# Optimization experiments

Measured on AMD Instinct MI355X. Metric: run time of the kernel, lower is better.

Reference implementation:

```python
import jax, jax.numpy as jnp
import numpy as np

B, C, H, W = 16, 256, 64, 64

def setup_inputs() -> dict:
    key = jax.random.key(0)
    ks = jax.random.split(key, 4)
    scale = 1.0 / np.sqrt(C)
    return {
        "x": jax.random.normal(ks[0], (B, C, H, W), dtype=jnp.float32),
        "w1": jax.random.normal(ks[1], (C, C), dtype=jnp.float32) * scale,
        "b1": jnp.zeros((C,), dtype=jnp.float32),
        "w2": jax.random.normal(ks[2], (C, C), dtype=jnp.float32) * scale,
        "b2": jnp.zeros((C,), dtype=jnp.float32),
        "w3": jax.random.normal(ks[3], (C, C), dtype=jnp.float32) * scale,
        "b3": jnp.zeros((C,), dtype=jnp.float32),
    }

def reference(x, w1, b1, w2, b2, w3, b3):
    b, c, h, w = x.shape
    n = h * w
    # 1x1 convs == per-pixel linear maps over channels; w has shape [C_out, C_in]
    def proj(wt, bias):
        return jnp.einsum('bchw,oc->bohw', x, wt) + bias[None, :, None, None]
    v = proj(w1, b1).reshape(b, c, n).transpose(0, 2, 1)   # [B, N, C]
    q = proj(w2, b2).reshape(b, c, n)                      # [B, C, N]
    k = proj(w3, b3).reshape(b, c, n)                      # [B, C, N]
    weight = jnp.einsum('bcn,bdn->bcd', q, k)              # [B, C, C]
    # global softmax over the entire flattened C*C matrix per batch element
    weight = jax.nn.softmax(weight.reshape(b, -1), axis=1).reshape(b, c, c)
    out = jnp.einsum('bnc,bcd->bdn', v, weight)            # [B, C, N]
    return out.reshape(x.shape)
```

## Files before the change

### kernel.cpp

```cpp
#include <hip/hip_runtime.h>


typedef unsigned short u16;
typedef __attribute__((ext_vector_type(8))) short short8;
typedef __attribute__((ext_vector_type(4))) float floatx4;

__device__ __forceinline__ u16 f2b(float f) {
  union { float f; unsigned int u; } v; v.f = f;
  unsigned int u = v.u;
  return (u16)((u + 0x7fffu + ((u >> 16) & 1u)) >> 16);
}
__device__ __forceinline__ float b2f(u16 h) {
  union { unsigned int u; float f; } v; v.u = ((unsigned int)h) << 16;
  return v.f;
}

__global__ __launch_bounds__(256) void prep_w_kernel(
    const float* __restrict__ w1, const float* __restrict__ w2, const float* __restrict__ w3,
    u16* __restrict__ W1Th, u16* __restrict__ W2h, u16* __restrict__ W2l,
    u16* __restrict__ W3h, u16* __restrict__ W3l) {
  const int blk = blockIdx.x, t = threadIdx.x;
  if (blk < 64) {
    __shared__ float tile[32][33];
    const int e0 = (blk & 7) * 32, c0 = (blk >> 3) * 32;
    const int tx = t & 31, ty = t >> 5;
#pragma unroll
    for (int i = 0; i < 4; ++i)
      tile[ty + i * 8][tx] = w1[(c0 + ty + i * 8) * 256 + e0 + tx];
    __syncthreads();
#pragma unroll
    for (int i = 0; i < 4; ++i)
      W1Th[(e0 + ty + i * 8) * 256 + c0 + tx] = f2b(tile[tx][ty + i * 8]);
  } else {
    const int i = (blk - 64) * 256 + t;
    const int e = i & 0xffff;
    const float f = (i >> 16) ? w3[e] : w2[e];
    u16 h = f2b(f);
    if (i >> 16) { W3h[e] = h; W3l[e] = f2b(f - b2f(h)); }
    else         { W2h[e] = h; W2l[e] = f2b(f - b2f(h)); }
  }
}

__global__ __launch_bounds__(512, 2) void gram_kernel(
    const float* __restrict__ x, float* __restrict__ Gp, float* __restrict__ xsum) {
  constexpr int LR = 40;
  __shared__ u16 lH[256 * LR], lL[256 * LR];
  const int b = blockIdx.x >> 4, s = blockIdx.x & 15;
  const float* Xb = x + (long)b * 1048576 + s * 256;
  const int t = threadIdx.x;
  const int lane = t & 63, wave = t >> 6;
  const int quad = lane >> 4, l16 = lane & 15;
  const int wm = (wave & 1) * 128, wn = (wave >> 1) * 64;
  floatx4 acc[8][4] = {};
  float xacc[2] = {0.f, 0.f};
  for (int kb = 0; kb < 256; kb += 32) {
    __syncthreads();
#pragma unroll
    for (int h = 0; h < 2; ++h) {
      const int item = t + h * 512;
      const int r = item >> 2, qc = (item & 3) * 8;
      const float4 f0 = *(const float4*)(Xb + (long)r * 4096 + kb + qc);
      const float4 f1 = *(const float4*)(Xb + (long)r * 4096 + kb + qc + 4);
      const float f[8] = {f0.x, f0.y, f0.z, f0.w, f1.x, f1.y, f1.z, f1.w};
      union { u16 h8[8]; uint4 q; } uh, ul;
#pragma unroll
      for (int i = 0; i < 8; ++i) {
        const u16 hi = f2b(f[i]);
        uh.h8[i] = hi;
        ul.h8[i] = f2b(f[i] - b2f(hi));
        xacc[h] += f[i];
      }
      *(uint4*)(lH + r * LR + qc) = uh.q;
      *(uint4*)(lL + r * LR + qc) = ul.q;
    }
    __syncthreads();
    short8 ah[8], al[8];
#pragma unroll
    for (int i = 0; i < 8; ++i) {
      ah[i] = *(const short8*)(lH + (wm + i * 16 + l16) * LR + quad * 8);
      al[i] = *(const short8*)(lL + (wm + i * 16 + l16) * LR + quad * 8);
    }
#pragma unroll
    for (int j = 0; j < 4; ++j) {
      const short8 bh = *(const short8*)(lH + (wn + j * 16 + l16) * LR + quad * 8);
      const short8 bl = *(const short8*)(lL + (wn + j * 16 + l16) * LR + quad * 8);
#pragma unroll
      for (int i = 0; i < 8; ++i) {
        acc[i][j] = __builtin_amdgcn_mfma_f32_16x16x32_bf16(ah[i], bh, acc[i][j], 0, 0, 0);
        acc[i][j] = __builtin_amdgcn_mfma_f32_16x16x32_bf16(ah[i], bl, acc[i][j], 0, 0, 0);
        acc[i][j] = __builtin_amdgcn_mfma_f32_16x16x32_bf16(al[i], bh, acc[i][j], 0, 0, 0);
      }
    }
  }
#pragma unroll
  for (int h = 0; h < 2; ++h) {
    float v = xacc[h];
    v += __shfl_xor(v, 1);
    v += __shfl_xor(v, 2);
    if ((t & 3) == 0) atomicAdd(&xsum[b * 256 + ((t + h * 512) >> 2)], v);
  }
  float* G = Gp + ((long)b * 16 + s) * 65536;
#pragma unroll
  for (int i = 0; i < 8; ++i) {
    const int row0 = wm + i * 16 + quad * 4;
#pragma unroll
    for (int j = 0; j < 4; ++j) {
      const int col = wn + j * 16 + l16;
#pragma unroll
      for (int r = 0; r < 4; ++r)
        G[(long)(row0 + r) * 256 + col] = acc[i][j][r];
    }
  }
}

__global__ void reduce_g_kernel(const float* __restrict__ Gp, u16* __restrict__ Gh,
                                u16* __restrict__ Gl) {
  const long e = (long)blockIdx.x * 256 + threadIdx.x;
  const long base = ((e >> 16) << 20) + (e & 65535);
  float s = 0.f;
#pragma unroll
  for (int i = 0; i < 16; ++i) s += Gp[base + (long)i * 65536];
  u16 h = f2b(s);
  Gh[e] = h;
  Gl[e] = f2b(s - b2f(h));
}

template <bool X3, int EPI>
__global__ __launch_bounds__(256) void gemm_tn(
    const u16* __restrict__ Ah, const u16* __restrict__ Al,
    const u16* __restrict__ Bh, const u16* __restrict__ Bl,
    long aBatch, long bBatch, long oBatch,
    int M, int N, int K, int tilesM,
    float* __restrict__ outF, u16* __restrict__ outH, u16* __restrict__ outL) {
  constexpr int LR = 40;
  __shared__ u16 smem[(X3 ? 4 : 2) * 128 * LR];
  u16* lAh = smem;
  u16* lBh = smem + 128 * LR;
  u16* lAl = X3 ? (smem + 2 * 128 * LR) : nullptr;
  u16* lBl = X3 ? (smem + 3 * 128 * LR) : nullptr;

  const int b = blockIdx.z;
  const int tm = blockIdx.x % tilesM, tn = blockIdx.x / tilesM;
  const u16* Ahb = Ah + (long)b * aBatch;
  const u16* Bhb = Bh + (long)b * bBatch;
  const u16* Alb = X3 ? (Al + (long)b * aBatch) : nullptr;
  const u16* Blb = X3 ? (Bl + (long)b * bBatch) : nullptr;

  const int t = threadIdx.x;
  const int lane = t & 63, wave = t >> 6;
  const int quad = lane >> 4, l16 = lane & 15;
  const int wm = (wave & 1) * 64, wn = (wave >> 1) * 64;
  const int srow = t >> 2, scol = (t & 3) * 8;

  floatx4 acc[4][4] = {};

  for (int kk = 0; kk < K; kk += 32) {
    __syncthreads();
#pragma unroll
    for (int h = 0; h < 2; ++h) {
      const int r = srow + h * 64;
      *(uint4*)(lAh + r * LR + scol) = *(const uint4*)(Ahb + (long)(tm * 128 + r) * K + kk + scol);
      *(uint4*)(lBh + r * LR + scol) = *(const uint4*)(Bhb + (long)(tn * 128 + r) * K + kk + scol);
      if (X3) {
        *(uint4*)(lAl + r * LR + scol) = *(const uint4*)(Alb + (long)(tm * 128 + r) * K + kk + scol);
        *(uint4*)(lBl + r * LR + scol) = *(const uint4*)(Blb + (long)(tn * 128 + r) * K + kk + scol);
      }
    }
    __syncthreads();
    short8 afh[4], bfh[4], afl[4], bfl[4];
#pragma unroll
    for (int i = 0; i < 4; ++i) {
      afh[i] = *(const short8*)(lAh + (wm + i * 16 + l16) * LR + quad * 8);
      bfh[i] = *(const short8*)(lBh + (wn + i * 16 + l16) * LR + quad * 8);
      if (X3) {
        afl[i] = *(const short8*)(lAl + (wm + i * 16 + l16) * LR + quad * 8);
        bfl[i] = *(const short8*)(lBl + (wn + i * 16 + l16) * LR + quad * 8);
      }
    }
#pragma unroll
    for (int i = 0; i < 4; ++i)
#pragma unroll
      for (int j = 0; j < 4; ++j) {
        acc[i][j] = __builtin_amdgcn_mfma_f32_16x16x32_bf16(afh[i], bfh[j], acc[i][j], 0, 0, 0);
        if (X3) {
          acc[i][j] = __builtin_amdgcn_mfma_f32_16x16x32_bf16(afh[i], bfl[j], acc[i][j], 0, 0, 0);
          acc[i][j] = __builtin_amdgcn_mfma_f32_16x16x32_bf16(afl[i], bfh[j], acc[i][j], 0, 0, 0);
        }
      }
  }

  const long obase = (long)b * oBatch;
#pragma unroll
  for (int i = 0; i < 4; ++i) {
    const int mb = tm * 128 + wm + i * 16 + quad * 4;
#pragma unroll
    for (int j = 0; j < 4; ++j) {
      const int n = tn * 128 + wn + j * 16 + l16;
#pragma unroll
      for (int r = 0; r < 4; ++r) {
        const float v = acc[i][j][r];
        const long idx = obase + (long)(mb + r) * N + n;
        if (EPI == 0) {
          outF[idx] = v;
        } else if (EPI == 1) {
          u16 h = f2b(v);
          outH[idx] = h;
          outL[idx] = f2b(v - b2f(h));
        } else {
          outH[idx] = f2b(v);
        }
      }
    }
  }
}

__global__ __launch_bounds__(256) void gemm_out(
    const u16* __restrict__ Mh, const float* __restrict__ x,
    const float* __restrict__ bb, float* __restrict__ out) {
  constexpr int LR = 40;
  __shared__ u16 lA[128 * LR], lB[128 * LR];
  const int b = blockIdx.z;
  const int tm = blockIdx.x & 1, tn = blockIdx.x >> 1;
  const u16* Ab = Mh + (long)b * 65536;
  const float* Xb = x + (long)b * 1048576 + tn * 128;
  const int t = threadIdx.x;
  const int lane = t & 63, wave = t >> 6;
  const int quad = lane >> 4, l16 = lane & 15;
  const int wm = (wave & 1) * 64, wn = (wave >> 1) * 64;
  const int erp = (t >> 4) * 2;
  const int n0 = (t & 15) * 8;
  floatx4 acc[4][4] = {};
  for (int kk = 0; kk < 256; kk += 32) {
    __syncthreads();
#pragma unroll
    for (int h = 0; h < 2; ++h) {
      const int r = (t >> 2) + h * 64;
      *(uint4*)(lA + r * LR + (t & 3) * 8) =
          *(const uint4*)(Ab + (long)(tm * 128 + r) * 256 + kk + (t & 3) * 8);
    }
    {
      const float4 a0 = *(const float4*)(Xb + (long)(kk + erp) * 4096 + n0);
      const float4 a1 = *(const float4*)(Xb + (long)(kk + erp) * 4096 + n0 + 4);
      const float4 c0 = *(const float4*)(Xb + (long)(kk + erp + 1) * 4096 + n0);
      const float4 c1 = *(const float4*)(Xb + (long)(kk + erp + 1) * 4096 + n0 + 4);
      const float fa[8] = {a0.x, a0.y, a0.z, a0.w, a1.x, a1.y, a1.z, a1.w};
      const float fc[8] = {c0.x, c0.y, c0.z, c0.w, c1.x, c1.y, c1.z, c1.w};
#pragma unroll
      for (int i = 0; i < 8; ++i) {
        const int nl = n0 + i;
        const int sb = (erp >> 3) ^ ((nl >> 4) & 3);
        const unsigned int pk =
            (unsigned int)f2b(fa[i]) | ((unsigned int)f2b(fc[i]) << 16);
        *(unsigned int*)(lB + nl * LR + sb * 8 + (erp & 7)) = pk;
      }
    }
    __syncthreads();
    short8 af[4], bf[4];
#pragma unroll
    for (int i = 0; i < 4; ++i) {
      af[i] = *(const short8*)(lA + (wm + i * 16 + l16) * LR + quad * 8);
      const int n = wn + i * 16 + l16;
      const int rb = quad ^ ((n >> 4) & 3);
      bf[i] = *(const short8*)(lB + n * LR + rb * 8);
    }
#pragma unroll
    for (int i = 0; i < 4; ++i)
#pragma unroll
      for (int j = 0; j < 4; ++j)
        acc[i][j] = __builtin_amdgcn_mfma_f32_16x16x32_bf16(af[i], bf[j], acc[i][j], 0, 0, 0);
  }
  const long obase = (long)b * 1048576;
#pragma unroll
  for (int i = 0; i < 4; ++i) {
    const int mb = tm * 128 + wm + i * 16 + quad * 4;
#pragma unroll
    for (int j = 0; j < 4; ++j) {
      const int n = tn * 128 + wn + j * 16 + l16;
#pragma unroll
      for (int r = 0; r < 4; ++r)
        out[obase + (long)(mb + r) * 4096 + n] = acc[i][j][r] + bb[b * 256 + mb + r];
    }
  }
}

__global__ __launch_bounds__(512) void bias_prep_kernel(
    const float* __restrict__ w2, const float* __restrict__ w3,
    const float* __restrict__ xsum, float* __restrict__ S2, float* __restrict__ S3) {
  __shared__ float xs[256];
  const int b = blockIdx.x, t = threadIdx.x;
  if (t < 256) xs[t] = xsum[b * 256 + t];
  __syncthreads();
  const float* wm = (t < 256) ? w2 : w3;
  const int a = t & 255;
  float s = 0.f;
#pragma unroll 4
  for (int c = 0; c < 256; ++c) s += wm[a * 256 + c] * xs[c];
  if (t < 256) S2[b * 256 + a] = s;
  else         S3[b * 256 + a] = s;
}

__global__ __launch_bounds__(256) void softmax_pass1(
    const float* __restrict__ Lt, const float* __restrict__ S2, const float* __restrict__ S3,
    const float* __restrict__ b2, const float* __restrict__ b3,
    float* __restrict__ bm, float* __restrict__ bs) {
  __shared__ float ls2[256], lb2[256];
  __shared__ float redm[4], reds[4];
  const int b = blockIdx.y, blk = blockIdx.x, t = threadIdx.x;
  ls2[t] = S2[b * 256 + t];
  lb2[t] = b2[t];
  __syncthreads();
  const int fw0 = blk * 2048 + t * 8;
  const int d = fw0 >> 8, a0 = fw0 & 255;
  const float c1 = b3[d];
  const float c0 = S3[b * 256 + d] + 4096.f * c1;
  const long base = (long)b * 65536 + fw0;
  float4 v0 = *(const float4*)(Lt + base);
  float4 v1 = *(const float4*)(Lt + base + 4);
  float v[8] = {v0.x, v0.y, v0.z, v0.w, v1.x, v1.y, v1.z, v1.w};
  float m = -3.4e38f;
#pragma unroll
  for (int i = 0; i < 8; ++i) {
    v[i] += lb2[a0 + i] * c0 + c1 * ls2[a0 + i];
    m = fmaxf(m, v[i]);
  }
  for (int o = 32; o; o >>= 1) m = fmaxf(m, __shfl_xor(m, o));
  const int wid = t >> 6, lane = t & 63;
  if (lane == 0) redm[wid] = m;
  __syncthreads();
  const float bmax = fmaxf(fmaxf(redm[0], redm[1]), fmaxf(redm[2], redm[3]));
  float s = 0.f;
#pragma unroll
  for (int i = 0; i < 8; ++i) s += __expf(v[i] - bmax);
  for (int o = 32; o; o >>= 1) s += __shfl_xor(s, o);
  if (lane == 0) reds[wid] = s;
  __syncthreads();
  if (t == 0) {
    bm[b * 32 + blk] = bmax;
    bs[b * 32 + blk] = reds[0] + reds[1] + reds[2] + reds[3];
  }
}

__global__ __launch_bounds__(256) void softmax_pass3(
    const float* __restrict__ Lt, const float* __restrict__ S2, const float* __restrict__ S3,
    const float* __restrict__ b2, const float* __restrict__ b3,
    const float* __restrict__ bm, const float* __restrict__ bs,
    u16* __restrict__ WTh) {
  __shared__ float ls2[256], lb2[256];
  __shared__ float sM, sInv;
  const int b = blockIdx.y, blk = blockIdx.x, t = threadIdx.x;
  if (t < 64) {
    const float m = (t < 32) ? bm[b * 32 + t] : -3.4e38f;
    float s = (t < 32) ? bs[b * 32 + t] : 0.f;
    float M = m;
    for (int o = 32; o; o >>= 1) M = fmaxf(M, __shfl_xor(M, o));
    s *= __expf(m - M);
    for (int o = 32; o; o >>= 1) s += __shfl_xor(s, o);
    if (t == 0) { sM = M; sInv = 1.0f / s; }
  }
  ls2[t] = S2[b * 256 + t];
  lb2[t] = b2[t];
  __syncthreads();
  const float M = sM, inv = sInv;
  const int fw0 = blk * 2048 + t * 8;
  const int d = fw0 >> 8, a0 = fw0 & 255;
  const float c1 = b3[d];
  const float c0 = S3[b * 256 + d] + 4096.f * c1;
  const long base = (long)b * 65536 + fw0;
  float4 v0 = *(const float4*)(Lt + base);
  float4 v1 = *(const float4*)(Lt + base + 4);
  float v[8] = {v0.x, v0.y, v0.z, v0.w, v1.x, v1.y, v1.z, v1.w};
  union { u16 h[8]; uint4 q; } o;
#pragma unroll
  for (int i = 0; i < 8; ++i) {
    const float vv = v[i] + lb2[a0 + i] * c0 + c1 * ls2[a0 + i];
    o.h[i] = f2b(__expf(vv - M) * inv);
  }
  *(uint4*)(WTh + base) = o.q;
}

__global__ void bb_kernel(const u16* __restrict__ WTh, const float* __restrict__ b1,
                          float* __restrict__ bb) {
  const int b = blockIdx.x, d = threadIdx.x;
  const u16* row = WTh + (long)b * 65536 + d * 256;
  float s = 0.f;
#pragma unroll 4
  for (int c = 0; c < 256; ++c) s += b2f(row[c]) * b1[c];
  bb[b * 256 + d] = s;
}

extern "C" void kernel_launch(void* const* d_in, const int* in_sizes, int n_in,
                              void* d_out, int out_size, void* d_ws, size_t ws_size,
                              hipStream_t stream) {
  const float* x  = (const float*)d_in[0];
  const float* w1 = (const float*)d_in[1];
  const float* b1 = (const float*)d_in[2];
  const float* w2 = (const float*)d_in[3];
  const float* b2 = (const float*)d_in[4];
  const float* w3 = (const float*)d_in[5];
  const float* b3 = (const float*)d_in[6];
  float* out = (float*)d_out;

  char* ws = (char*)d_ws;
  size_t off = 0;
  auto alloc = [&](size_t bytes) {
    void* p = ws + off;
    off += (bytes + 255) & ~(size_t)255;
    return p;
  };
  float* Gp = (float*)alloc(16ull * 16 * 65536 * 4);
  u16* Gh   = (u16*)alloc(16ull * 65536 * 2);
  u16* Gl   = (u16*)alloc(16ull * 65536 * 2);
  u16* T3h  = (u16*)alloc(16ull * 65536 * 2);
  u16* T3l  = (u16*)alloc(16ull * 65536 * 2);
  float* Lb = (float*)alloc(16ull * 65536 * 4);
  u16* WTh  = (u16*)alloc(16ull * 65536 * 2);
  u16* Mh   = (u16*)alloc(16ull * 65536 * 2);
  u16* W1Th = (u16*)alloc(65536 * 2);
  u16* W2h  = (u16*)alloc(65536 * 2);
  u16* W2l  = (u16*)alloc(65536 * 2);
  u16* W3h  = (u16*)alloc(65536 * 2);
  u16* W3l  = (u16*)alloc(65536 * 2);
  float* xsum = (float*)alloc(16 * 256 * 4);
  float* S2   = (float*)alloc(16 * 256 * 4);
  float* S3   = (float*)alloc(16 * 256 * 4);
  float* bmx  = (float*)alloc(16 * 32 * 4);
  float* bsx  = (float*)alloc(16 * 32 * 4);
  float* bb   = (float*)alloc(16 * 256 * 4);

  hipMemsetAsync(xsum, 0, 16 * 256 * 4, stream);
  prep_w_kernel<<<576, 256, 0, stream>>>(w1, w2, w3, W1Th, W2h, W2l, W3h, W3l);

  gram_kernel<<<256, 512, 0, stream>>>(x, Gp, xsum);
  reduce_g_kernel<<<4096, 256, 0, stream>>>(Gp, Gh, Gl);

  gemm_tn<true, 1><<<dim3(4, 1, 16), 256, 0, stream>>>(
      W3h, W3l, Gh, Gl, 0, 65536, 65536,
      256, 256, 256, 2, nullptr, T3h, T3l);
  gemm_tn<true, 0><<<dim3(4, 1, 16), 256, 0, stream>>>(
      T3h, T3l, W2h, W2l, 65536, 0, 65536,
      256, 256, 256, 2, Lb, nullptr, nullptr);

  bias_prep_kernel<<<16, 512, 0, stream>>>(w2, w3, xsum, S2, S3);
  softmax_pass1<<<dim3(32, 16), 256, 0, stream>>>(Lb, S2, S3, b2, b3, bmx, bsx);
  softmax_pass3<<<dim3(32, 16), 256, 0, stream>>>(Lb, S2, S3, b2, b3, bmx, bsx, WTh);

  bb_kernel<<<16, 256, 0, stream>>>(WTh, b1, bb);
  gemm_tn<false, 2><<<dim3(4, 1, 16), 256, 0, stream>>>(
      WTh, nullptr, W1Th, nullptr, 65536, 0, 65536,
      256, 256, 256, 2, nullptr, Mh, nullptr);
  gemm_out<<<dim3(64, 1, 16), 256, 0, stream>>>(Mh, x, bb, out);
}
```

Baseline: 253.9 us.

## Double-buffer gram kernel LDS staging and shrink small GEMM tiles to 64x64

```diff
diff --git a/kernel.cpp b/kernel.cpp
--- a/kernel.cpp
+++ b/kernel.cpp
@@ -41,63 +41,82 @@
   }
 }
 
+__device__ __forceinline__ void stage8(const float4 a, const float4 b,
+                                       u16* dH, u16* dL, float& xa) {
+  const float f[8] = {a.x, a.y, a.z, a.w, b.x, b.y, b.z, b.w};
+  union { u16 h8[8]; uint4 q; } uh, ul;
+#pragma unroll
+  for (int i = 0; i < 8; ++i) {
+    const u16 hi = f2b(f[i]);
+    uh.h8[i] = hi;
+    ul.h8[i] = f2b(f[i] - b2f(hi));
+    xa += f[i];
+  }
+  *(uint4*)dH = uh.q;
+  *(uint4*)dL = ul.q;
+}
+
 __global__ __launch_bounds__(512, 2) void gram_kernel(
     const float* __restrict__ x, float* __restrict__ Gp, float* __restrict__ xsum) {
   constexpr int LR = 40;
-  __shared__ u16 lH[256 * LR], lL[256 * LR];
+  __shared__ u16 lH[2][256 * LR], lL[2][256 * LR];
   const int b = blockIdx.x >> 4, s = blockIdx.x & 15;
   const float* Xb = x + (long)b * 1048576 + s * 256;
   const int t = threadIdx.x;
   const int lane = t & 63, wave = t >> 6;
   const int quad = lane >> 4, l16 = lane & 15;
   const int wm = (wave & 1) * 128, wn = (wave >> 1) * 64;
+  const int r0 = t >> 2, qc = (t & 3) * 8;
+  const int r1 = r0 + 128;
   floatx4 acc[8][4] = {};
-  float xacc[2] = {0.f, 0.f};
-  for (int kb = 0; kb < 256; kb += 32) {
-    __syncthreads();
-#pragma unroll
-    for (int h = 0; h < 2; ++h) {
-      const int item = t + h * 512;
-      const int r = item >> 2, qc = (item & 3) * 8;
-      const float4 f0 = *(const float4*)(Xb + (long)r * 4096 + kb + qc);
-      const float4 f1 = *(const float4*)(Xb + (long)r * 4096 + kb + qc + 4);
-      const float f[8] = {f0.x, f0.y, f0.z, f0.w, f1.x, f1.y, f1.z, f1.w};
-      union { u16 h8[8]; uint4 q; } uh, ul;
+  float xa0 = 0.f, xa1 = 0.f;
+  float4 p[4];
+  p[0] = *(const float4*)(Xb + (long)r0 * 4096 + qc);
+  p[1] = *(const float4*)(Xb + (long)r0 * 4096 + qc + 4);
+  p[2] = *(const float4*)(Xb + (long)r1 * 4096 + qc);
+  p[3] = *(const float4*)(Xb + (long)r1 * 4096 + qc + 4);
+  stage8(p[0], p[1], lH[0] + r0 * LR + qc, lL[0] + r0 * LR + qc, xa0);
+  stage8(p[2], p[3], lH[0] + r1 * LR + qc, lL[0] + r1 * LR + qc, xa1);
+  __syncthreads();
+  for (int kb = 0; kb < 8; ++kb) {
+    const int cur = kb & 1, nxt = cur ^ 1;
+    if (kb < 7) {
+      const long kk = (kb + 1) * 32;
+      p[0] = *(const float4*)(Xb + (long)r0 * 4096 + kk + qc);
+      p[1] = *(const float4*)(Xb + (long)r0 * 4096 + kk + qc + 4);
+      p[2] = *(const float4*)(Xb + (long)r1 * 4096 + kk + qc);
+      p[3] = *(const float4*)(Xb + (long)r1 * 4096 + kk + qc + 4);
+    }
+    const u16* cH = lH[cur];
+    const u16* cL = lL[cur];
+#pragma unroll
+    for (int j = 0; j < 4; ++j) {
+      const short8 bh = *(const short8*)(cH + (wn + j * 16 + l16) * LR + quad * 8);
+      const short8 bl = *(const short8*)(cL + (wn + j * 16 + l16) * LR + quad * 8);
 #pragma unroll
       for (int i = 0; i < 8; ++i) {
-        const u16 hi = f2b(f[i]);
-        uh.h8[i] = hi;
-        ul.h8[i] = f2b(f[i] - b2f(hi));
-        xacc[h] += f[i];
+        const short8 ah = *(const short8*)(cH + (wm + i * 16 + l16) * LR + quad * 8);
+        const short8 al = *(const short8*)(cL + (wm + i * 16 + l16) * LR + quad * 8);
+        acc[i][j] = __builtin_amdgcn_mfma_f32_16x16x32_bf16(ah, bh, acc[i][j], 0, 0, 0);
+        acc[i][j] = __builtin_amdgcn_mfma_f32_16x16x32_bf16(ah, bl, acc[i][j], 0, 0, 0);
+        acc[i][j] = __builtin_amdgcn_mfma_f32_16x16x32_bf16(al, bh, acc[i][j], 0, 0, 0);
       }
-      *(uint4*)(lH + r * LR + qc) = uh.q;
-      *(uint4*)(lL + r * LR + qc) = ul.q;
-    }
-    __syncthreads();
-    short8 ah[8], al[8];
-#pragma unroll
-    for (int i = 0; i < 8; ++i) {
-      ah[i] = *(const short8*)(lH + (wm + i * 16 + l16) * LR + quad * 8);
-      al[i] = *(const short8*)(lL + (wm + i * 16 + l16) * LR + quad * 8);
-    }
-#pragma unroll
-    for (int j = 0; j < 4; ++j) {
-      const short8 bh = *(const short8*)(lH + (wn + j * 16 + l16) * LR + quad * 8);
-      const short8 bl = *(const short8*)(lL + (wn + j * 16 + l16) * LR + quad * 8);
-#pragma unroll
-      for (int i = 0; i < 8; ++i) {
-        acc[i][j] = __builtin_amdgcn_mfma_f32_16x16x32_bf16(ah[i], bh, acc[i][j], 0, 0, 0);
-        acc[i][j] = __builtin_amdgcn_mfma_f32_16x16x32_bf16(ah[i], bl, acc[i][j], 0, 0, 0);
-        acc[i][j] = __builtin_amdgcn_mfma_f32_16x16x32_bf16(al[i], bh, acc[i][j], 0, 0, 0);
-      }
-    }
-  }
-#pragma unroll
-  for (int h = 0; h < 2; ++h) {
-    float v = xacc[h];
+    }
+    if (kb < 7) {
+      stage8(p[0], p[1], lH[nxt] + r0 * LR + qc, lL[nxt] + r0 * LR + qc, xa0);
+      stage8(p[2], p[3], lH[nxt] + r1 * LR + qc, lL[nxt] + r1 * LR + qc, xa1);
+    }
+    __syncthreads();
+  }
+  {
+    float v = xa0;
     v += __shfl_xor(v, 1);
     v += __shfl_xor(v, 2);
-    if ((t & 3) == 0) atomicAdd(&xsum[b * 256 + ((t + h * 512) >> 2)], v);
+    if ((t & 3) == 0) atomicAdd(&xsum[b * 256 + r0], v);
+    v = xa1;
+    v += __shfl_xor(v, 1);
+    v += __shfl_xor(v, 2);
+    if ((t & 3) == 0) atomicAdd(&xsum[b * 256 + r1], v);
   }
   float* G = Gp + ((long)b * 16 + s) * 65536;
 #pragma unroll
@@ -126,50 +145,41 @@
 }
 
 template <bool X3, int EPI>
-__global__ __launch_bounds__(256) void gemm_tn(
+__global__ __launch_bounds__(256) void gemm_small(
     const u16* __restrict__ Ah, const u16* __restrict__ Al,
     const u16* __restrict__ Bh, const u16* __restrict__ Bl,
     long aBatch, long bBatch, long oBatch,
-    int M, int N, int K, int tilesM,
     float* __restrict__ outF, u16* __restrict__ outH, u16* __restrict__ outL) {
   constexpr int LR = 40;
-  __shared__ u16 smem[(X3 ? 4 : 2) * 128 * LR];
+  __shared__ u16 smem[(X3 ? 4 : 2) * 64 * LR];
   u16* lAh = smem;
-  u16* lBh = smem + 128 * LR;
-  u16* lAl = X3 ? (smem + 2 * 128 * LR) : nullptr;
-  u16* lBl = X3 ? (smem + 3 * 128 * LR) : nullptr;
-
+  u16* lBh = smem + 64 * LR;
+  u16* lAl = X3 ? (smem + 2 * 64 * LR) : nullptr;
+  u16* lBl = X3 ? (smem + 3 * 64 * LR) : nullptr;
   const int b = blockIdx.z;
-  const int tm = blockIdx.x % tilesM, tn = blockIdx.x / tilesM;
-  const u16* Ahb = Ah + (long)b * aBatch;
-  const u16* Bhb = Bh + (long)b * bBatch;
-  const u16* Alb = X3 ? (Al + (long)b * aBatch) : nullptr;
-  const u16* Blb = X3 ? (Bl + (long)b * bBatch) : nullptr;
-
+  const int tm = blockIdx.x & 3, tn = blockIdx.x >> 2;
+  const u16* Ahb = Ah + (long)b * aBatch + (long)tm * 64 * 256;
+  const u16* Bhb = Bh + (long)b * bBatch + (long)tn * 64 * 256;
+  const u16* Alb = X3 ? (Al + (long)b * aBatch + (long)tm * 64 * 256) : nullptr;
+  const u16* Blb = X3 ? (Bl + (long)b * bBatch + (long)tn * 64 * 256) : nullptr;
   const int t = threadIdx.x;
   const int lane = t & 63, wave = t >> 6;
   const int quad = lane >> 4, l16 = lane & 15;
-  const int wm = (wave & 1) * 64, wn = (wave >> 1) * 64;
-  const int srow = t >> 2, scol = (t & 3) * 8;
-
-  floatx4 acc[4][4] = {};
-
-  for (int kk = 0; kk < K; kk += 32) {
-    __syncthreads();
-#pragma unroll
-    for (int h = 0; h < 2; ++h) {
-      const int r = srow + h * 64;
-      *(uint4*)(lAh + r * LR + scol) = *(const uint4*)(Ahb + (long)(tm * 128 + r) * K + kk + scol);
-      *(uint4*)(lBh + r * LR + scol) = *(const uint4*)(Bhb + (long)(tn * 128 + r) * K + kk + scol);
-      if (X3) {
-        *(uint4*)(lAl + r * LR + scol) = *(const uint4*)(Alb + (long)(tm * 128 + r) * K + kk + scol);
-        *(uint4*)(lBl + r * LR + scol) = *(const uint4*)(Blb + (long)(tn * 128 + r) * K + kk + scol);
-      }
-    }
-    __syncthreads();
-    short8 afh[4], bfh[4], afl[4], bfl[4];
-#pragma unroll
-    for (int i = 0; i < 4; ++i) {
+  const int wm = (wave & 1) * 32, wn = (wave >> 1) * 32;
+  const int r = t >> 2, qc = (t & 3) * 8;
+  floatx4 acc[2][2] = {};
+  for (int kk = 0; kk < 256; kk += 32) {
+    __syncthreads();
+    *(uint4*)(lAh + r * LR + qc) = *(const uint4*)(Ahb + (long)r * 256 + kk + qc);
+    *(uint4*)(lBh + r * LR + qc) = *(const uint4*)(Bhb + (long)r * 256 + kk + qc);
+    if (X3) {
+      *(uint4*)(lAl + r * LR + qc) = *(const uint4*)(Alb + (long)r * 256 + kk + qc);
+      *(uint4*)(lBl + r * LR + qc) = *(const uint4*)(Blb + (long)r * 256 + kk + qc);
+    }
+    __syncthreads();
+    short8 afh[2], bfh[2], afl[2], bfl[2];
+#pragma unroll
+    for (int i = 0; i < 2; ++i) {
       afh[i] = *(const short8*)(lAh + (wm + i * 16 + l16) * LR + quad * 8);
       bfh[i] = *(const short8*)(lBh + (wn + i * 16 + l16) * LR + quad * 8);
       if (X3) {
@@ -178,9 +188,9 @@
       }
     }
 #pragma unroll
-    for (int i = 0; i < 4; ++i)
-#pragma unroll
-      for (int j = 0; j < 4; ++j) {
+    for (int i = 0; i < 2; ++i)
+#pragma unroll
+      for (int j = 0; j < 2; ++j) {
         acc[i][j] = __builtin_amdgcn_mfma_f32_16x16x32_bf16(afh[i], bfh[j], acc[i][j], 0, 0, 0);
         if (X3) {
           acc[i][j] = __builtin_amdgcn_mfma_f32_16x16x32_bf16(afh[i], bfl[j], acc[i][j], 0, 0, 0);
@@ -188,18 +198,17 @@
         }
       }
   }
-
   const long obase = (long)b * oBatch;
 #pragma unroll
-  for (int i = 0; i < 4; ++i) {
-    const int mb = tm * 128 + wm + i * 16 + quad * 4;
-#pragma unroll
-    for (int j = 0; j < 4; ++j) {
-      const int n = tn * 128 + wn + j * 16 + l16;
-#pragma unroll
-      for (int r = 0; r < 4; ++r) {
-        const float v = acc[i][j][r];
-        const long idx = obase + (long)(mb + r) * N + n;
+  for (int i = 0; i < 2; ++i) {
+    const int mb = tm * 64 + wm + i * 16 + quad * 4;
+#pragma unroll
+    for (int j = 0; j < 2; ++j) {
+      const int n = tn * 64 + wn + j * 16 + l16;
+#pragma unroll
+      for (int rr = 0; rr < 4; ++rr) {
+        const float v = acc[i][j][rr];
+        const long idx = obase + (long)(mb + rr) * 256 + n;
         if (EPI == 0) {
           outF[idx] = v;
         } else if (EPI == 1) {
@@ -433,20 +442,17 @@
   gram_kernel<<<256, 512, 0, stream>>>(x, Gp, xsum);
   reduce_g_kernel<<<4096, 256, 0, stream>>>(Gp, Gh, Gl);
 
-  gemm_tn<true, 1><<<dim3(4, 1, 16), 256, 0, stream>>>(
-      W3h, W3l, Gh, Gl, 0, 65536, 65536,
-      256, 256, 256, 2, nullptr, T3h, T3l);
-  gemm_tn<true, 0><<<dim3(4, 1, 16), 256, 0, stream>>>(
-      T3h, T3l, W2h, W2l, 65536, 0, 65536,
-      256, 256, 256, 2, Lb, nullptr, nullptr);
+  gemm_small<true, 1><<<dim3(16, 1, 16), 256, 0, stream>>>(
+      W3h, W3l, Gh, Gl, 0, 65536, 65536, nullptr, T3h, T3l);
+  gemm_small<true, 0><<<dim3(16, 1, 16), 256, 0, stream>>>(
+      T3h, T3l, W2h, W2l, 65536, 0, 65536, Lb, nullptr, nullptr);
 
   bias_prep_kernel<<<16, 512, 0, stream>>>(w2, w3, xsum, S2, S3);
   softmax_pass1<<<dim3(32, 16), 256, 0, stream>>>(Lb, S2, S3, b2, b3, bmx, bsx);
   softmax_pass3<<<dim3(32, 16), 256, 0, stream>>>(Lb, S2, S3, b2, b3, bmx, bsx, WTh);
 
   bb_kernel<<<16, 256, 0, stream>>>(WTh, b1, bb);
-  gemm_tn<false, 2><<<dim3(4, 1, 16), 256, 0, stream>>>(
-      WTh, nullptr, W1Th, nullptr, 65536, 0, 65536,
-      256, 256, 256, 2, nullptr, Mh, nullptr);
+  gemm_small<false, 2><<<dim3(16, 1, 16), 256, 0, stream>>>(
+      WTh, nullptr, W1Th, nullptr, 65536, 0, 65536, nullptr, Mh, nullptr);
   gemm_out<<<dim3(64, 1, 16), 256, 0, stream>>>(Mh, x, bb, out);
 }
```

Result: faster. 239.0 us (-5.9%).
